# Performance work log

Measured on AMD Instinct MI355X. Metric: run time of the kernel, lower is better.

## Reference

```python
import jax, jax.numpy as jnp
import numpy as np

B, S, HID = 2, 2048, 2048
NH, NKV = 16, 4
HD = HID // NH  # 128
GROUPS = NH // NKV


def _rope(x, cos, sin):
    # x: [B, S, H, D]; cos/sin: [S, D//2]
    xr = x.reshape(*x.shape[:-1], HD // 2, 2)
    x0, x1 = xr[..., 0], xr[..., 1]
    c = cos[None, :, None, :]
    s = sin[None, :, None, :]
    o0 = x0 * c - x1 * s
    o1 = x0 * s + x1 * c
    return jnp.stack([o0, o1], axis=-1).reshape(*x.shape)


def setup_inputs() -> dict:
    key = jax.random.key(0)
    k1, k2, k3, k4, k5, k6 = jax.random.split(key, 6)
    hidden_states = jax.random.normal(k1, (B, S, HID), dtype=jnp.float32)
    # RoPE frequencies (llama-style)
    inv_freq = 1.0 / (10000.0 ** (np.arange(0, HD, 2, dtype=np.float32) / HD))
    t = np.arange(S, dtype=np.float32)
    ang = np.outer(t, inv_freq)  # [S, HD//2]
    freqs_cos = jnp.asarray(np.cos(ang), dtype=jnp.float32)
    freqs_sin = jnp.asarray(np.sin(ang), dtype=jnp.float32)
    # additive causal mask [1,1,S,S]
    causal = jnp.triu(jnp.full((S, S), -1e9, dtype=jnp.float32), k=1)
    attention_mask = causal[None, None]
    sc = 0.02
    Wq = jax.random.normal(k2, (NH * HD, HID), dtype=jnp.float32) * sc
    Wk = jax.random.normal(k3, (NKV * HD, HID), dtype=jnp.float32) * sc
    Wv = jax.random.normal(k4, (NKV * HD, HID), dtype=jnp.float32) * sc
    Wo = jax.random.normal(k5, (HID, NH * HD), dtype=jnp.float32) * sc
    return {"hidden_states": hidden_states, "freqs_cos": freqs_cos,
            "freqs_sin": freqs_sin, "attention_mask": attention_mask,
            "Wq": Wq, "Wk": Wk, "Wv": Wv, "Wo": Wo}


def reference(hidden_states, freqs_cos, freqs_sin, attention_mask, Wq, Wk, Wv, Wo):
    xq = (hidden_states @ Wq.T).reshape(B, S, NH, HD)
    xk = (hidden_states @ Wk.T).reshape(B, S, NKV, HD)
    xv = (hidden_states @ Wv.T).reshape(B, S, NKV, HD)
    xq = _rope(xq, freqs_cos, freqs_sin)
    xk = _rope(xk, freqs_cos, freqs_sin)
    # expand KV heads for GQA: [B,S,NKV,D] -> [B,S,NH,D]
    xk = jnp.repeat(xk, GROUPS, axis=2)
    xv = jnp.repeat(xv, GROUPS, axis=2)
    q = xq.transpose(0, 2, 1, 3)  # [B,H,S,D]
    k = xk.transpose(0, 2, 1, 3)
    v = xv.transpose(0, 2, 1, 3)
    scores = jnp.einsum('bhqd,bhkd->bhqk', q, k) / jnp.sqrt(jnp.float32(HD))
    scores = scores + attention_mask
    probs = jax.nn.softmax(scores, axis=-1)
    out = jnp.einsum('bhqk,bhkd->bhqd', probs, v)
    out = out.transpose(0, 2, 1, 3).reshape(B, S, NH * HD)
    return out @ Wo.T
```

## Files before the change

### kernel.cpp

```cpp
#include <hip/hip_runtime.h>


typedef __attribute__((ext_vector_type(8))) short bf16x8;
typedef __attribute__((ext_vector_type(4))) float f32x4;
typedef __attribute__((ext_vector_type(16))) float f32x16;
typedef __attribute__((ext_vector_type(4))) unsigned short u16x4;
typedef unsigned short u16;

#define B_   2
#define S_   2048
#define HID_ 2048
#define NH_  16
#define NKV_ 4
#define HD_  128

__device__ __forceinline__ u16 f2bf(float f) {
  unsigned u = __float_as_uint(f);
  u = (u + 0x7FFFu + ((u >> 16) & 1u)) >> 16;
  return (u16)u;
}
__device__ __forceinline__ float bf2f(u16 h) {
  return __uint_as_float(((unsigned)h) << 16);
}

__device__ __forceinline__ void gl_lds16(const void* g, void* l) {
  __builtin_amdgcn_global_load_lds(
      (const __attribute__((address_space(1))) void*)g,
      (__attribute__((address_space(3))) void*)l, 16, 0, 0);
}

__global__ void convert_bf16(const float* __restrict__ src, u16* __restrict__ dst, int n8) {
  int i = blockIdx.x * 256 + threadIdx.x;
  if (i >= n8) return;
  const float4* s = (const float4*)src + (size_t)i * 2;
  float4 a = s[0], b = s[1];
  union { u16 u[8]; uint4 v; } o;
  o.u[0] = f2bf(a.x); o.u[1] = f2bf(a.y); o.u[2] = f2bf(a.z); o.u[3] = f2bf(a.w);
  o.u[4] = f2bf(b.x); o.u[5] = f2bf(b.y); o.u[6] = f2bf(b.z); o.u[7] = f2bf(b.w);
  ((uint4*)dst)[i] = o.v;
}

template<int EPI>
__launch_bounds__(256, 2)
__global__ void gemm128(const u16* __restrict__ A, const u16* __restrict__ Bm,
                        float* __restrict__ C, u16* __restrict__ Qb,
                        u16* __restrict__ Kb, u16* __restrict__ Vb,
                        int N, int K)
{
  __shared__ u16 As[128 * 64];
  __shared__ u16 Bs[128 * 64];
  const int tid = threadIdx.x;
  const int lane = tid & 63;
  const int w = tid >> 6;
  const int lo = lane & 15, hi = lane >> 4;
  const int wr = w >> 1, wc = w & 1;
  const int rowA0 = blockIdx.x * 128;
  const int rowB0 = blockIdx.y * 128;

  f32x4 acc[4][4] = {};

  for (int kt = 0; kt < K; kt += 64) {
    __syncthreads();
#pragma unroll
    for (int it = 0; it < 4; ++it) {
      int c = it * 256 + tid;
      int r = c >> 3;
      int cb = (c & 7) * 8;
      gl_lds16(A + (size_t)(rowA0 + r) * K + kt + cb, (char*)As + c * 16);
      gl_lds16(Bm + (size_t)(rowB0 + r) * K + kt + cb, (char*)Bs + c * 16);
    }
    __syncthreads();
#pragma unroll
    for (int kk = 0; kk < 64; kk += 32) {
      bf16x8 af[4], bfr[4];
#pragma unroll
      for (int m = 0; m < 4; ++m)
        af[m] = *(const bf16x8*)(As + (wr * 64 + m * 16 + lo) * 64 + kk + hi * 8);
#pragma unroll
      for (int n = 0; n < 4; ++n)
        bfr[n] = *(const bf16x8*)(Bs + (wc * 64 + n * 16 + lo) * 64 + kk + hi * 8);
#pragma unroll
      for (int m = 0; m < 4; ++m)
#pragma unroll
        for (int n = 0; n < 4; ++n)
          acc[m][n] = __builtin_amdgcn_mfma_f32_16x16x32_bf16(af[m], bfr[n], acc[m][n], 0, 0, 0);
    }
  }

#pragma unroll
  for (int m = 0; m < 4; ++m) {
#pragma unroll
    for (int n = 0; n < 4; ++n) {
#pragma unroll
      for (int r = 0; r < 4; ++r) {
        int grow = rowA0 + wr * 64 + m * 16 + hi * 4 + r;
        int gcol = rowB0 + wc * 64 + n * 16 + lo;
        float v = acc[m][n][r];
        if (EPI == 0) {
          C[(size_t)grow * N + gcol] = v;
        } else {
          int bb = grow >> 11, s = grow & 2047;
          u16 hv = f2bf(v);
          if (gcol < 2048) {
            int h = gcol >> 7, d = gcol & 127;
            Qb[(((size_t)bb * NH_ + h) * S_ + s) * HD_ + d] = hv;
          } else if (gcol < 2560) {
            int h = (gcol - 2048) >> 7, d = gcol & 127;
            Kb[(((size_t)bb * NKV_ + h) * S_ + s) * HD_ + d] = hv;
          } else {
            int h = (gcol - 2560) >> 7, d = gcol & 127;
            Vb[(((size_t)bb * NKV_ + h) * S_ + s) * HD_ + d] = hv;
          }
        }
      }
    }
  }
}

__global__ void rope_k(u16* __restrict__ Qb, u16* __restrict__ Kb,
                       const float* __restrict__ fcos, const float* __restrict__ fsin)
{
  int idx = blockIdx.x * 256 + threadIdx.x;
  int chunk = idx & 15;
  int s = (idx >> 4) & 2047;
  int hs = idx >> 15;
  u16* p = (hs < 32) ? (Qb + ((size_t)hs * S_ + s) * HD_ + chunk * 8)
                     : (Kb + ((size_t)(hs - 32) * S_ + s) * HD_ + chunk * 8);
  uint4 raw = *(uint4*)p;
  float4 c4 = *(const float4*)(fcos + (size_t)s * 64 + chunk * 4);
  float4 s4 = *(const float4*)(fsin + (size_t)s * 64 + chunk * 4);
  float cc[4] = {c4.x, c4.y, c4.z, c4.w};
  float ss[4] = {s4.x, s4.y, s4.z, s4.w};
  unsigned* rw = (unsigned*)&raw;
#pragma unroll
  for (int j = 0; j < 4; ++j) {
    float x0 = bf2f((u16)(rw[j] & 0xFFFFu));
    float x1 = bf2f((u16)(rw[j] >> 16));
    float o0 = x0 * cc[j] - x1 * ss[j];
    float o1 = x0 * ss[j] + x1 * cc[j];
    rw[j] = (unsigned)f2bf(o0) | ((unsigned)f2bf(o1) << 16);
  }
  *(uint4*)p = raw;
}

__global__ void transpose_v(const u16* __restrict__ Vb, u16* __restrict__ Vtg)
{
  __shared__ u16 t[64][65];
  const int st = blockIdx.x, dt = blockIdx.y, hs = blockIdx.z;
  const u16* src = Vb + ((size_t)hs * S_ + st * 64) * HD_ + dt * 64;
#pragma unroll
  for (int it = 0; it < 2; ++it) {
    int c = it * 256 + threadIdx.x;
    int r = c >> 3, cb = (c & 7) * 8;
    uint4 v = *(const uint4*)(src + (size_t)r * HD_ + cb);
    u16* u = (u16*)&v;
#pragma unroll
    for (int e = 0; e < 8; ++e) t[r][cb + e] = u[e];
  }
  __syncthreads();
#pragma unroll
  for (int it = 0; it < 2; ++it) {
    int c = it * 256 + threadIdx.x;
    int r2 = c >> 3, cb2 = (c & 7) * 8;
    union { u16 u[8]; uint4 v; } o;
#pragma unroll
    for (int e = 0; e < 8; ++e) o.u[e] = t[cb2 + e][r2];
    *(uint4*)(Vtg + ((size_t)hs * HD_ + dt * 64 + r2) * S_ + st * 64 + cb2) = o.v;
  }
}

__launch_bounds__(512, 2)
__global__ void flash_attn(const u16* __restrict__ Qb, const u16* __restrict__ Kb,
                           const u16* __restrict__ Vtg, u16* __restrict__ AO)
{
  __shared__ u16 Ks[2][64 * 128];
  __shared__ u16 Vt[2][128 * 64];

  const int tid = threadIdx.x, lane = tid & 63, w = tid >> 6;
  const int ql = lane & 31, hh = lane >> 5;
  const int h = blockIdx.y, b = blockIdx.z, kvh = h >> 2;
  const u16* Qh = Qb + ((size_t)b * NH_ + h) * S_ * HD_;
  const u16* Kh = Kb + ((size_t)b * NKV_ + kvh) * S_ * HD_;
  const u16* Vh = Vtg + ((size_t)b * NKV_ + kvh) * HD_ * S_;
  const float cf = 0.12752704581383682f;
  const float NEG = -30000.f;

  for (int pass = 0; pass < 2; ++pass) {
    const int qb = pass ? (7 - (int)blockIdx.x) : (int)blockIdx.x;
    const int q0w = qb * 256 + w * 32;
    const int qg = q0w + ql;
    const int nt = qb * 4 + 4;

    bf16x8 qf[8];
#pragma unroll
    for (int s = 0; s < 8; ++s)
      qf[s] = *(const bf16x8*)(Qh + (size_t)qg * HD_ + s * 16 + hh * 8);

    f32x16 o[4] = {};
    float m = NEG, l = 0.f;

    __syncthreads();
#pragma unroll
    for (int it = 0; it < 2; ++it) {
      int ck = it * 512 + tid; int r = ck >> 4; int slot = (ck & 15) ^ (r & 7);
      gl_lds16(Kh + (size_t)r * HD_ + slot * 8, (char*)Ks[0] + ck * 16);
    }
#pragma unroll
    for (int it = 0; it < 2; ++it) {
      int cv = it * 512 + tid; int r = cv >> 3; int slot = (cv & 7) ^ (r & 7);
      gl_lds16(Vh + (size_t)r * S_ + slot * 8, (char*)Vt[0] + cv * 16);
    }
    __syncthreads();
    int cur = 0;

    for (int t = 0; t < nt; ++t) {
      if (t < nt - 1) {
        const int kn = (t + 1) * 64;
#pragma unroll
        for (int it = 0; it < 2; ++it) {
          int ck = it * 512 + tid; int r = ck >> 4; int slot = (ck & 15) ^ (r & 7);
          gl_lds16(Kh + (size_t)(kn + r) * HD_ + slot * 8, (char*)Ks[cur ^ 1] + ck * 16);
        }
#pragma unroll
        for (int it = 0; it < 2; ++it) {
          int cv = it * 512 + tid; int r = cv >> 3; int slot = (cv & 7) ^ (r & 7);
          gl_lds16(Vh + (size_t)r * S_ + kn + slot * 8, (char*)Vt[cur ^ 1] + cv * 16);
        }
      }
      const int kt = t * 64;
      if (kt < q0w + 32) {
        f32x16 st[2] = {};
        __builtin_amdgcn_s_setprio(1);
#pragma unroll
        for (int sl = 0; sl < 8; ++sl) {
          int slot = ((2 * sl + hh) ^ (ql & 7)) * 16;
          bf16x8 k0 = *(const bf16x8*)((const char*)Ks[cur] + ql * 256 + slot);
          bf16x8 k1 = *(const bf16x8*)((const char*)Ks[cur] + (32 + ql) * 256 + slot);
          st[0] = __builtin_amdgcn_mfma_f32_32x32x16_bf16(k0, qf[sl], st[0], 0, 0, 0);
          st[1] = __builtin_amdgcn_mfma_f32_32x32x16_bf16(k1, qf[sl], st[1], 0, 0, 0);
        }
        __builtin_amdgcn_s_setprio(0);

        if ((kt + 63) > q0w) {
#pragma unroll
          for (int i = 0; i < 2; ++i)
#pragma unroll
            for (int r = 0; r < 16; ++r) {
              int kv = kt + 32 * i + (r & 3) + 8 * (r >> 2) + 4 * hh;
              if (kv > qg) st[i][r] = NEG;
            }
        }

        float mx[8];
#pragma unroll
        for (int r = 0; r < 8; ++r)
          mx[r] = fmaxf(fmaxf(st[0][r], st[0][r + 8]), fmaxf(st[1][r], st[1][r + 8]));
#pragma unroll
        for (int d = 4; d > 0; d >>= 1)
#pragma unroll
          for (int r = 0; r < d; ++r) mx[r] = fmaxf(mx[r], mx[r + d]);
        float tmax = fmaxf(mx[0], __shfl_xor(mx[0], 32));

        float mn = fmaxf(m, tmax);
        float rs = __builtin_exp2f((m - mn) * cf);
        m = mn; l *= rs;
#pragma unroll
        for (int dt = 0; dt < 4; ++dt)
#pragma unroll
          for (int r = 0; r < 16; ++r) o[dt][r] *= rs;

        const float mc = m * cf;
#pragma unroll
        for (int i = 0; i < 2; ++i)
#pragma unroll
          for (int r = 0; r < 16; ++r)
            st[i][r] = __builtin_exp2f(__builtin_fmaf(st[i][r], cf, -mc));
        float sm[8];
#pragma unroll
        for (int r = 0; r < 8; ++r)
          sm[r] = (st[0][r] + st[0][r + 8]) + (st[1][r] + st[1][r + 8]);
#pragma unroll
        for (int d = 4; d > 0; d >>= 1)
#pragma unroll
          for (int r = 0; r < d; ++r) sm[r] += sm[r + d];
        l += sm[0] + __shfl_xor(sm[0], 32);

        bf16x8 pb[4];
#pragma unroll
        for (int i = 0; i < 2; ++i)
#pragma unroll
          for (int s = 0; s < 2; ++s) {
            unsigned wA, wC, wB, wD;
            asm("v_cvt_pk_bf16_f32 %0, %1, %2" : "=v"(wA) : "v"(st[i][8*s+0]), "v"(st[i][8*s+1]));
            asm("v_cvt_pk_bf16_f32 %0, %1, %2" : "=v"(wC) : "v"(st[i][8*s+2]), "v"(st[i][8*s+3]));
            asm("v_cvt_pk_bf16_f32 %0, %1, %2" : "=v"(wB) : "v"(st[i][8*s+4]), "v"(st[i][8*s+5]));
            asm("v_cvt_pk_bf16_f32 %0, %1, %2" : "=v"(wD) : "v"(st[i][8*s+6]), "v"(st[i][8*s+7]));
            unsigned tA = (unsigned)__shfl_xor((int)wA, 32);
            unsigned tB = (unsigned)__shfl_xor((int)wB, 32);
            unsigned tC = (unsigned)__shfl_xor((int)wC, 32);
            unsigned tD = (unsigned)__shfl_xor((int)wD, 32);
            union { unsigned u[4]; bf16x8 v; } pk;
            pk.u[0] = hh ? tB : wA;
            pk.u[1] = hh ? tD : wC;
            pk.u[2] = hh ? wB : tA;
            pk.u[3] = hh ? wD : tC;
            pb[2 * i + s] = pk.v;
          }

        __builtin_amdgcn_s_setprio(1);
#pragma unroll
        for (int dt = 0; dt < 4; ++dt)
#pragma unroll
          for (int ks = 0; ks < 4; ++ks) {
            int row = 32 * dt + ql;
            bf16x8 vf = *(const bf16x8*)((const char*)Vt[cur] + row * 128 +
                                         (((2 * ks + hh) ^ (ql & 7)) * 16));
            o[dt] = __builtin_amdgcn_mfma_f32_32x32x16_bf16(vf, pb[ks], o[dt], 0, 0, 0);
          }
        __builtin_amdgcn_s_setprio(0);
      }
      __syncthreads();
      cur ^= 1;
    }

    const float inv = 1.f / l;
#pragma unroll
    for (int dt = 0; dt < 4; ++dt)
#pragma unroll
      for (int g = 0; g < 4; ++g) {
        u16x4 pk4;
#pragma unroll
        for (int e = 0; e < 4; ++e) pk4[e] = f2bf(o[dt][4 * g + e] * inv);
        *(u16x4*)(AO + ((size_t)b * S_ + qg) * HID_ + h * HD_ + 32 * dt + 8 * g + 4 * hh) = pk4;
      }
  }
}

extern "C" void kernel_launch(void* const* d_in, const int* in_sizes, int n_in,
                              void* d_out, int out_size, void* d_ws, size_t ws_size,
                              hipStream_t stream)
{
  (void)in_sizes; (void)n_in; (void)out_size; (void)ws_size;
  const float* X  = (const float*)d_in[0];
  const float* fc = (const float*)d_in[1];
  const float* fs = (const float*)d_in[2];
  const float* Wq = (const float*)d_in[4];
  const float* Wk = (const float*)d_in[5];
  const float* Wv = (const float*)d_in[6];
  const float* Wo = (const float*)d_in[7];
  float* out = (float*)d_out;

  u16* Xb  = (u16*)d_ws;
  u16* Wb  = Xb + (size_t)4096 * 2048;
  u16* Qb  = Wb + (size_t)3072 * 2048;
  u16* Kb  = Qb + (size_t)B_ * NH_ * S_ * HD_;
  u16* Vb  = Kb + (size_t)B_ * NKV_ * S_ * HD_;
  u16* AO  = Xb;
  u16* Wob = Wb;
  u16* Vtg = Wb + (size_t)2048 * 2048;

  convert_bf16<<<4096, 256, 0, stream>>>(X,  Xb,               4096 * 2048 / 8);
  convert_bf16<<<2048, 256, 0, stream>>>(Wq, Wb,               2048 * 2048 / 8);
  convert_bf16<<<512,  256, 0, stream>>>(Wk, Wb + 2048 * 2048, 512 * 2048 / 8);
  convert_bf16<<<512,  256, 0, stream>>>(Wv, Wb + 2560 * 2048, 512 * 2048 / 8);

  gemm128<1><<<dim3(32, 24), 256, 0, stream>>>(Xb, Wb, nullptr, Qb, Kb, Vb, 3072, 2048);

  convert_bf16<<<2048, 256, 0, stream>>>(Wo, Wob, 2048 * 2048 / 8);

  transpose_v<<<dim3(32, 2, 8), 256, 0, stream>>>(Vb, Vtg);

  rope_k<<<5120, 256, 0, stream>>>(Qb, Kb, fc, fs);

  flash_attn<<<dim3(4, NH_, B_), 512, 0, stream>>>(Qb, Kb, Vtg, AO);

  gemm128<0><<<dim3(32, 16), 256, 0, stream>>>(AO, Wob, out, nullptr, nullptr, nullptr, 2048, 2048);
}
```

Measured before the change: 266.0 us.

## Shrink flash-attention blocks to two waves and quadruple the grid

```diff
diff --git a/kernel.cpp b/kernel.cpp
--- a/kernel.cpp
+++ b/kernel.cpp
@@ -169,7 +169,7 @@
   }
 }
 
-__launch_bounds__(512, 2)
+__launch_bounds__(128, 2)
 __global__ void flash_attn(const u16* __restrict__ Qb, const u16* __restrict__ Kb,
                            const u16* __restrict__ Vtg, u16* __restrict__ AO)
 {
@@ -178,6 +178,7 @@
 
   const int tid = threadIdx.x, lane = tid & 63, w = tid >> 6;
   const int ql = lane & 31, hh = lane >> 5;
+  const int swl = (ql & 7) ^ ((ql >> 3) & 3);
   const int h = blockIdx.y, b = blockIdx.z, kvh = h >> 2;
   const u16* Qh = Qb + ((size_t)b * NH_ + h) * S_ * HD_;
   const u16* Kh = Kb + ((size_t)b * NKV_ + kvh) * S_ * HD_;
@@ -185,11 +186,28 @@
   const float cf = 0.12752704581383682f;
   const float NEG = -30000.f;
 
+  auto STAGE = [&](int buf, int kt) {
+#pragma unroll
+    for (int it = 0; it < 8; ++it) {
+      int c = it * 128 + tid;
+      int r = c >> 4;
+      int slot = (c & 15) ^ (r & 7) ^ ((r >> 3) & 3);
+      gl_lds16(Kh + (size_t)(kt + r) * HD_ + slot * 8, (char*)Ks[buf] + c * 16);
+    }
+#pragma unroll
+    for (int it = 0; it < 8; ++it) {
+      int c = it * 128 + tid;
+      int r = c >> 3;
+      int slot = (c & 7) ^ ((r & 7) ^ ((r >> 3) & 3));
+      gl_lds16(Vh + (size_t)r * S_ + kt + slot * 8, (char*)Vt[buf] + c * 16);
+    }
+  };
+
   for (int pass = 0; pass < 2; ++pass) {
-    const int qb = pass ? (7 - (int)blockIdx.x) : (int)blockIdx.x;
-    const int q0w = qb * 256 + w * 32;
+    const int qb = pass ? (31 - (int)blockIdx.x) : (int)blockIdx.x;
+    const int q0w = qb * 64 + w * 32;
     const int qg = q0w + ql;
-    const int nt = qb * 4 + 4;
+    const int nt = qb + 1;
 
     bf16x8 qf[8];
 #pragma unroll
@@ -200,40 +218,19 @@
     float m = NEG, l = 0.f;
 
     __syncthreads();
-#pragma unroll
-    for (int it = 0; it < 2; ++it) {
-      int ck = it * 512 + tid; int r = ck >> 4; int slot = (ck & 15) ^ (r & 7);
-      gl_lds16(Kh + (size_t)r * HD_ + slot * 8, (char*)Ks[0] + ck * 16);
-    }
-#pragma unroll
-    for (int it = 0; it < 2; ++it) {
-      int cv = it * 512 + tid; int r = cv >> 3; int slot = (cv & 7) ^ (r & 7);
-      gl_lds16(Vh + (size_t)r * S_ + slot * 8, (char*)Vt[0] + cv * 16);
-    }
+    STAGE(0, 0);
     __syncthreads();
     int cur = 0;
 
     for (int t = 0; t < nt; ++t) {
-      if (t < nt - 1) {
-        const int kn = (t + 1) * 64;
-#pragma unroll
-        for (int it = 0; it < 2; ++it) {
-          int ck = it * 512 + tid; int r = ck >> 4; int slot = (ck & 15) ^ (r & 7);
-          gl_lds16(Kh + (size_t)(kn + r) * HD_ + slot * 8, (char*)Ks[cur ^ 1] + ck * 16);
-        }
-#pragma unroll
-        for (int it = 0; it < 2; ++it) {
-          int cv = it * 512 + tid; int r = cv >> 3; int slot = (cv & 7) ^ (r & 7);
-          gl_lds16(Vh + (size_t)r * S_ + kn + slot * 8, (char*)Vt[cur ^ 1] + cv * 16);
-        }
-      }
+      if (t < nt - 1) STAGE(cur ^ 1, (t + 1) * 64);
       const int kt = t * 64;
       if (kt < q0w + 32) {
         f32x16 st[2] = {};
         __builtin_amdgcn_s_setprio(1);
 #pragma unroll
         for (int sl = 0; sl < 8; ++sl) {
-          int slot = ((2 * sl + hh) ^ (ql & 7)) * 16;
+          int slot = ((2 * sl + hh) ^ swl) * 16;
           bf16x8 k0 = *(const bf16x8*)((const char*)Ks[cur] + ql * 256 + slot);
           bf16x8 k1 = *(const bf16x8*)((const char*)Ks[cur] + (32 + ql) * 256 + slot);
           st[0] = __builtin_amdgcn_mfma_f32_32x32x16_bf16(k0, qf[sl], st[0], 0, 0, 0);
@@ -314,7 +311,7 @@
           for (int ks = 0; ks < 4; ++ks) {
             int row = 32 * dt + ql;
             bf16x8 vf = *(const bf16x8*)((const char*)Vt[cur] + row * 128 +
-                                         (((2 * ks + hh) ^ (ql & 7)) * 16));
+                                         (((2 * ks + hh) ^ swl) & 7) * 16);
             o[dt] = __builtin_amdgcn_mfma_f32_32x32x16_bf16(vf, pb[ks], o[dt], 0, 0, 0);
           }
         __builtin_amdgcn_s_setprio(0);
@@ -372,7 +369,7 @@
 
   rope_k<<<5120, 256, 0, stream>>>(Qb, Kb, fc, fs);
 
-  flash_attn<<<dim3(4, NH_, B_), 512, 0, stream>>>(Qb, Kb, Vtg, AO);
+  flash_attn<<<dim3(16, NH_, B_), 128, 0, stream>>>(Qb, Kb, Vtg, AO);
 
   gemm128<0><<<dim3(32, 16), 256, 0, stream>>>(AO, Wob, out, nullptr, nullptr, nullptr, 2048, 2048);
 }
```

New measurement: 240.2 us. -9.7%, faster.
